# Optimization experiments

Hardware: AMD Instinct MI355X
Metric: run time of the kernel (lower is better)

## Reference

```python
import jax, jax.numpy as jnp
import numpy as np

W_BIT = 4
OUT_F = 11008
IN_F = 4096
K = 16


def unpack_sign(q_bytes):
    """q_bytes: [n_bytes] int32 holding uint8 values. Little-endian bit order.
    Returns float32 signs in {-1, +1} of shape [OUT_F, IN_F]."""
    bits = (q_bytes[:, None] >> jnp.arange(8, dtype=q_bytes.dtype)) & 1  # [n_bytes, 8]
    signs = (2 * bits - 1).astype(jnp.float32)
    return signs.reshape(OUT_F, IN_F)


def setup_inputs() -> dict:
    key = jax.random.key(0)
    k0, k1, k2, k3 = jax.random.split(key, 4)
    x = jax.random.normal(k0, (4, 2048, IN_F), dtype=jnp.float32)
    # packed sign bits: one byte stores 8 signs; OUT_F*IN_F//8 bytes per bit-plane
    qweight = jax.random.randint(k1, (W_BIT, OUT_F * IN_F // 8), 0, 256, dtype=jnp.int32)
    u = jax.random.normal(k2, (W_BIT, OUT_F, K), dtype=jnp.float32) * 0.05
    vt = jax.random.normal(k3, (W_BIT, K, IN_F), dtype=jnp.float32) * 0.05
    return {"x": x, "qweight": qweight, "u": u, "vt": vt}


def reference(x, qweight, u, vt):
    # Reconstruct full weight: w = sum_i sign_i * (u_i @ vt_i), then GEMM x @ w.T.
    # Loop over the small fixed w_bit count to avoid holding all [OUT,IN] bit-planes at once.
    w = jnp.zeros((OUT_F, IN_F), dtype=x.dtype)
    for i in range(W_BIT):
        signs = unpack_sign(qweight[i])            # [OUT_F, IN_F]
        w = w + signs * (u[i] @ vt[i])             # rank-K reconstruction masked by signs
    return x @ w.T                                  # [B, S, OUT_F]
```

## Files before the change

kernel.cpp:

```cpp
#include <hip/hip_runtime.h>
#include <hip/hip_bf16.h>

#define W_BIT 4
#define OUT_F 11008
#define IN_F 4096
#define KRANK 16
#define M_DIM 8192
#define QW_PLANE (OUT_F * IN_F / 8)

#define N_DIM OUT_F
#define K_DIM IN_F
#define NT 64
#define NBN 43

typedef __attribute__((ext_vector_type(8))) short short8;
typedef __attribute__((ext_vector_type(4))) float f32x4;

__device__ __forceinline__ short f2bf(float f) {
    union { float f; unsigned u; } v;
    v.f = f;
    unsigned r = v.u + 0x7fffu + ((v.u >> 16) & 1u);
    return (short)(r >> 16);
}

__device__ __forceinline__ void async16(void* lds, const void* g) {
    __builtin_amdgcn_global_load_lds(
        (const __attribute__((address_space(1))) unsigned int*)g,
        (__attribute__((address_space(3))) unsigned int*)lds,
        16, 0, 0);
}

#define BAR() __builtin_amdgcn_s_barrier()
#define LGKM0() do { asm volatile("s_waitcnt lgkmcnt(0)" ::: "memory"); \
                     __builtin_amdgcn_sched_barrier(0); } while (0)
#define VM8() asm volatile("s_waitcnt vmcnt(8)" ::: "memory")
#define VM0() asm volatile("s_waitcnt vmcnt(0)" ::: "memory")
#define PRIO1() __builtin_amdgcn_s_setprio(1)
#define PRIO0() __builtin_amdgcn_s_setprio(0)
#define SBAR0() __builtin_amdgcn_sched_barrier(0)

__global__ __launch_bounds__(256) void convert_x_kernel(
    const float* __restrict__ x, short* __restrict__ xb) {
    int tid = blockIdx.x * blockDim.x + threadIdx.x;
    int stride = gridDim.x * blockDim.x;
    const int n8 = (M_DIM * IN_F) / 8;
    for (int i = tid; i < n8; i += stride) {
        f32x4 a = ((const f32x4*)x)[2 * i];
        f32x4 b = ((const f32x4*)x)[2 * i + 1];
        short8 o;
        o[0] = f2bf(a[0]); o[1] = f2bf(a[1]); o[2] = f2bf(a[2]); o[3] = f2bf(a[3]);
        o[4] = f2bf(b[0]); o[5] = f2bf(b[1]); o[6] = f2bf(b[2]); o[7] = f2bf(b[3]);
        ((short8*)xb)[i] = o;
    }
}

__global__ __launch_bounds__(256) void reconstruct_w_kernel(
    const int* __restrict__ qw, const float* __restrict__ u,
    const float* __restrict__ vt, short* __restrict__ wb) {
    __shared__ float vts[W_BIT][KRANK][128];
    __shared__ float us[W_BIT][KRANK][64];

    const int t = threadIdx.x;
    const int o0 = blockIdx.y * 64;
    const int c0 = blockIdx.x * 128;

    for (int idx = t; idx < W_BIT * KRANK * 128; idx += 256) {
        int i = idx >> 11;
        int rem = idx & 2047;
        int k = rem >> 7;
        int c = rem & 127;
        vts[i][k][c] = vt[(i * KRANK + k) * IN_F + c0 + c];
    }
    for (int idx = t; idx < W_BIT * KRANK * 64; idx += 256) {
        int i = idx >> 10;
        int rem = idx & 1023;
        int o = rem >> 4;
        int k = rem & 15;
        us[i][k][o] = u[((size_t)i * OUT_F + o0 + o) * KRANK + k];
    }
    __syncthreads();

    const int to = (t >> 4) * 4;
    const int tc = (t & 15) * 8;

    float wacc[4][8];
#pragma unroll
    for (int r = 0; r < 4; ++r)
#pragma unroll
        for (int c = 0; c < 8; ++c) wacc[r][c] = 0.f;

#pragma unroll
    for (int i = 0; i < W_BIT; ++i) {
        float dot[4][8];
#pragma unroll
        for (int r = 0; r < 4; ++r)
#pragma unroll
            for (int c = 0; c < 8; ++c) dot[r][c] = 0.f;

#pragma unroll
        for (int k = 0; k < KRANK; ++k) {
            f32x4 uv = *(const f32x4*)&us[i][k][to];
            f32x4 v0 = *(const f32x4*)&vts[i][k][tc];
            f32x4 v1 = *(const f32x4*)&vts[i][k][tc + 4];
#pragma unroll
            for (int r = 0; r < 4; ++r) {
#pragma unroll
                for (int c = 0; c < 4; ++c) {
                    dot[r][c]     += uv[r] * v0[c];
                    dot[r][c + 4] += uv[r] * v1[c];
                }
            }
        }
#pragma unroll
        for (int r = 0; r < 4; ++r) {
            unsigned byte = (unsigned)qw[i * QW_PLANE + (((o0 + to + r) * IN_F + c0 + tc) >> 3)];
#pragma unroll
            for (int c = 0; c < 8; ++c) {
                wacc[r][c] += ((byte >> c) & 1u) ? dot[r][c] : -dot[r][c];
            }
        }
    }

#pragma unroll
    for (int r = 0; r < 4; ++r) {
        short8 o8;
#pragma unroll
        for (int c = 0; c < 8; ++c) o8[c] = f2bf(wacc[r][c]);
        *(short8*)&wb[(size_t)(o0 + to + r) * IN_F + c0 + tc] = o8;
    }
}

__global__ __launch_bounds__(512, 2) void gemm256_kernel(
    const short* __restrict__ A, const short* __restrict__ B, float* __restrict__ C) {
    extern __shared__ short lds[];

    const int t = threadIdx.x;
    const int lane = t & 63, wid = t >> 6;
    const int wr = wid >> 2, wc = wid & 3;
    const int fr = lane & 15, fq = lane >> 4;

    const int bid = blockIdx.x;
    const int cpx = gridDim.x >> 3;
    const int swz = (bid & 7) * cpx + (bid >> 3);
    const int bm = swz / NBN, bn = swz % NBN;
    const long row0 = (long)bm * 256, col0 = (long)bn * 256;

    const int srow_b = t >> 3;
    const int scol = (((t & 7) ^ ((t >> 3) & 7)) << 3);
    const short* gA = A + (row0 + srow_b) * K_DIM + scol;
    const short* gB = B + (col0 + srow_b) * K_DIM + scol;
    const int ldst = t * 8;

    const int arow = (wr * 128 + fr) * 64;
    const int brow = (wc * 64 + fr) * 64;
    const int cswz = (fr & 7) << 3;
    const int colk0  = (fq << 3) ^ cswz;
    const int colk32 = (32 | (fq << 3)) ^ cswz;

    f32x4 acc[8][4];
#pragma unroll
    for (int m = 0; m < 8; ++m)
#pragma unroll
        for (int n = 0; n < 4; ++n) acc[m][n] = (f32x4)0.f;

    short8 af0[8], af1[8], bf0[4], bf1[4];

#define STAGE4(gp, base, ktcol)                                        \
    _Pragma("unroll") for (int l = 0; l < 4; ++l)                      \
        async16(&lds[(base) + ldst + l * 4096],                        \
                (gp) + (size_t)l * 64 * K_DIM + (ktcol))

#define LDA8(dst, base, colk)                                          \
    _Pragma("unroll") for (int m = 0; m < 8; ++m)                      \
        dst[m] = *(const short8*)&lds[(base) + arow + m * 1024 + (colk)]

#define LDB1(dst, n, base, colk)                                       \
    dst[n] = *(const short8*)&lds[(base) + 16384 + brow + (n) * 1024 + (colk)]

#define MF2(A8, B4, nlo)                                               \
    _Pragma("unroll") for (int m = 0; m < 8; ++m) {                    \
        acc[m][nlo] = __builtin_amdgcn_mfma_f32_16x16x32_bf16(         \
            A8[m], B4[nlo], acc[m][nlo], 0, 0, 0);                     \
        acc[m][(nlo) + 1] = __builtin_amdgcn_mfma_f32_16x16x32_bf16(   \
            A8[m], B4[(nlo) + 1], acc[m][(nlo) + 1], 0, 0, 0);         \
    }

    STAGE4(gA, 0, 0);
    STAGE4(gB, 16384, 0);
    STAGE4(gA, 32768, 64);
    STAGE4(gB, 32768 + 16384, 64);
    VM8();
    BAR();
    LDA8(af0, 0, colk0);
    LDB1(bf0, 0, 0, colk0); LDB1(bf0, 1, 0, colk0);
    LDB1(bf0, 2, 0, colk0); LDB1(bf0, 3, 0, colk0);

    for (int g = 0; g < NT; ++g) {
        const int ab  = (g & 1) * 32768;
        const int ab2 = ((g & 1) ^ 1) * 32768;
        const bool st2 = (g + 2 < NT);
        const bool rd1 = (g + 1 < NT);
        const size_t kt2 = (size_t)(g + 2) * 64;

        LDA8(af1, ab, colk32);
        LDB1(bf1, 0, ab, colk32);
        LDB1(bf1, 1, ab, colk32);
        BAR();
        LGKM0();
        PRIO1(); MF2(af0, bf0, 0); PRIO0();
        SBAR0();
        BAR();

        if (st2) STAGE4(gA, ab, kt2);
        LDB1(bf1, 2, ab, colk32);
        LDB1(bf1, 3, ab, colk32);
        BAR();
        LGKM0();
        PRIO1(); MF2(af0, bf0, 2); PRIO0();
        SBAR0();
        BAR();

        if (st2) STAGE4(gB, ab + 16384, kt2);
        BAR();
        PRIO1(); MF2(af1, bf1, 0); PRIO0();
        if (st2) { VM8(); } else { VM0(); }
        SBAR0();
        BAR();

        if (rd1) {
            LDA8(af0, ab2, colk0);
            LDB1(bf0, 0, ab2, colk0); LDB1(bf0, 1, ab2, colk0);
            LDB1(bf0, 2, ab2, colk0); LDB1(bf0, 3, ab2, colk0);
        }
        BAR();
        LGKM0();
        PRIO1(); MF2(af1, bf1, 2); PRIO0();
        SBAR0();
        BAR();
    }

#pragma unroll
    for (int m = 0; m < 8; ++m) {
#pragma unroll
        for (int n = 0; n < 4; ++n) {
            f32x4 v = acc[m][n];
            long r0 = row0 + wr * 128 + m * 16 + fq * 4;
            long cc = col0 + wc * 64 + n * 16 + fr;
#pragma unroll
            for (int jj = 0; jj < 4; ++jj)
                C[(size_t)(r0 + jj) * N_DIM + cc] = v[jj];
        }
    }
#undef STAGE4
#undef LDA8
#undef LDB1
#undef MF2
}

extern "C" void kernel_launch(void* const* d_in, const int* in_sizes, int n_in,
                              void* d_out, int out_size, void* d_ws, size_t ws_size,
                              hipStream_t stream) {
    const float* x  = (const float*)d_in[0];
    const int*   qw = (const int*)d_in[1];
    const float* u  = (const float*)d_in[2];
    const float* vt = (const float*)d_in[3];
    float* out = (float*)d_out;

    const size_t wb_bytes = (size_t)OUT_F * IN_F * 2;
    short* wb = (short*)d_ws;
    short* xb = (short*)((char*)d_ws + wb_bytes);

    (void)hipFuncSetAttribute((const void*)gemm256_kernel,
                              hipFuncAttributeMaxDynamicSharedMemorySize, 131072);

    hipLaunchKernelGGL(convert_x_kernel, dim3(2048), dim3(256), 0, stream, x, xb);
    hipLaunchKernelGGL(reconstruct_w_kernel, dim3(IN_F / 128, OUT_F / 64), dim3(256), 0, stream,
                       qw, u, vt, wb);
    hipLaunchKernelGGL(gemm256_kernel, dim3((M_DIM / 256) * (N_DIM / 256)), dim3(512), 131072,
                       stream, xb, wb, out);
}
```

Before: 915.9 us.

## Restructure GEMM main loop into quadrant MFMA phases with staggered A/B prefetch

Reorganizes the bf16 GEMM inner loop into four phases, each issuing a 4x4 MFMA quadrant from smaller A and B register fragments. A is now prefetched one tile ahead into the other LDS buffer and B two tiles ahead. LDS waits use partial lgkmcnt counts instead of full drains, so fragment loads for the next phase overlap the current MFMAs. The goal is better overlap of LDS reads and global-to-LDS copies with the matrix units. In exchange, the asymmetric buffer timing adds hazard risk if the vmcnt and lgkmcnt counts are wrong.

```diff
diff --git a/kernel.cpp b/kernel.cpp
--- a/kernel.cpp
+++ b/kernel.cpp
@@ -31,13 +31,13 @@
 }
 
 #define BAR() __builtin_amdgcn_s_barrier()
-#define LGKM0() do { asm volatile("s_waitcnt lgkmcnt(0)" ::: "memory"); \
+#define SBAR0() __builtin_amdgcn_sched_barrier(0)
+#define LGKM(n) do { asm volatile("s_waitcnt lgkmcnt(" #n ")" ::: "memory"); \
                      __builtin_amdgcn_sched_barrier(0); } while (0)
-#define VM8() asm volatile("s_waitcnt vmcnt(8)" ::: "memory")
-#define VM0() asm volatile("s_waitcnt vmcnt(0)" ::: "memory")
+#define VMC(n) do { asm volatile("s_waitcnt vmcnt(" #n ")" ::: "memory"); \
+                    __builtin_amdgcn_sched_barrier(0); } while (0)
 #define PRIO1() __builtin_amdgcn_s_setprio(1)
 #define PRIO0() __builtin_amdgcn_s_setprio(0)
-#define SBAR0() __builtin_amdgcn_sched_barrier(0)
 
 __global__ __launch_bounds__(256) void convert_x_kernel(
     const float* __restrict__ x, short* __restrict__ xb) {
@@ -163,78 +163,75 @@
 #pragma unroll
         for (int n = 0; n < 4; ++n) acc[m][n] = (f32x4)0.f;
 
-    short8 af0[8], af1[8], bf0[4], bf1[4];
+    short8 af[4][4], bf[2][4];
 
 #define STAGE4(gp, base, ktcol)                                        \
     _Pragma("unroll") for (int l = 0; l < 4; ++l)                      \
         async16(&lds[(base) + ldst + l * 4096],                        \
                 (gp) + (size_t)l * 64 * K_DIM + (ktcol))
 
-#define LDA8(dst, base, colk)                                          \
-    _Pragma("unroll") for (int m = 0; m < 8; ++m)                      \
-        dst[m] = *(const short8*)&lds[(base) + arow + m * 1024 + (colk)]
-
-#define LDB1(dst, n, base, colk)                                       \
-    dst[n] = *(const short8*)&lds[(base) + 16384 + brow + (n) * 1024 + (colk)]
-
-#define MF2(A8, B4, nlo)                                               \
-    _Pragma("unroll") for (int m = 0; m < 8; ++m) {                    \
-        acc[m][nlo] = __builtin_amdgcn_mfma_f32_16x16x32_bf16(         \
-            A8[m], B4[nlo], acc[m][nlo], 0, 0, 0);                     \
-        acc[m][(nlo) + 1] = __builtin_amdgcn_mfma_f32_16x16x32_bf16(   \
-            A8[m], B4[(nlo) + 1], acc[m][(nlo) + 1], 0, 0, 0);         \
-    }
+#define LDA4(j, base, mh, colk)                                        \
+    _Pragma("unroll") for (int m = 0; m < 4; ++m)                      \
+        af[j][m] = *(const short8*)&lds[(base) + arow + (mh) * 4096 + m * 1024 + (colk)]
+
+#define LDB4(j, base, colk)                                            \
+    _Pragma("unroll") for (int n = 0; n < 4; ++n)                      \
+        bf[j][n] = *(const short8*)&lds[(base) + 16384 + brow + n * 1024 + (colk)]
+
+#define MFQ(j, jb, mbase)                                              \
+    _Pragma("unroll") for (int m = 0; m < 4; ++m)                      \
+        _Pragma("unroll") for (int n = 0; n < 4; ++n)                  \
+            acc[(mbase) + m][n] = __builtin_amdgcn_mfma_f32_16x16x32_bf16( \
+                af[j][m], bf[jb][n], acc[(mbase) + m][n], 0, 0, 0)
 
     STAGE4(gA, 0, 0);
     STAGE4(gB, 16384, 0);
-    STAGE4(gA, 32768, 64);
     STAGE4(gB, 32768 + 16384, 64);
-    VM8();
+    VMC(4);
     BAR();
-    LDA8(af0, 0, colk0);
-    LDB1(bf0, 0, 0, colk0); LDB1(bf0, 1, 0, colk0);
-    LDB1(bf0, 2, 0, colk0); LDB1(bf0, 3, 0, colk0);
+    LDA4(0, 0, 0, colk0);
+    LDB4(0, 0, colk0);
 
     for (int g = 0; g < NT; ++g) {
-        const int ab  = (g & 1) * 32768;
-        const int ab2 = ((g & 1) ^ 1) * 32768;
-        const bool st2 = (g + 2 < NT);
-        const bool rd1 = (g + 1 < NT);
-        const size_t kt2 = (size_t)(g + 2) * 64;
-
-        LDA8(af1, ab, colk32);
-        LDB1(bf1, 0, ab, colk32);
-        LDB1(bf1, 1, ab, colk32);
-        BAR();
-        LGKM0();
-        PRIO1(); MF2(af0, bf0, 0); PRIO0();
-        SBAR0();
-        BAR();
-
-        if (st2) STAGE4(gA, ab, kt2);
-        LDB1(bf1, 2, ab, colk32);
-        LDB1(bf1, 3, ab, colk32);
-        BAR();
-        LGKM0();
-        PRIO1(); MF2(af0, bf0, 2); PRIO0();
-        SBAR0();
-        BAR();
-
-        if (st2) STAGE4(gB, ab + 16384, kt2);
-        BAR();
-        PRIO1(); MF2(af1, bf1, 0); PRIO0();
-        if (st2) { VM8(); } else { VM0(); }
-        SBAR0();
-        BAR();
-
-        if (rd1) {
-            LDA8(af0, ab2, colk0);
-            LDB1(bf0, 0, ab2, colk0); LDB1(bf0, 1, ab2, colk0);
-            LDB1(bf0, 2, ab2, colk0); LDB1(bf0, 3, ab2, colk0);
-        }
-        BAR();
-        LGKM0();
-        PRIO1(); MF2(af1, bf1, 2); PRIO0();
+        const int cur = (g & 1) * 32768;
+        const int oth = 32768 - cur;
+        const bool h1 = (g + 1 < NT);
+        const bool h2 = (g + 2 < NT);
+
+        if (h1) STAGE4(gA, oth, (size_t)(g + 1) * 64);
+        LDA4(1, cur, 1, colk0);
+        BAR();
+        LGKM(4);
+        PRIO1(); MFQ(0, 0, 0); PRIO0();
+        SBAR0();
+        BAR();
+
+        LDA4(2, cur, 0, colk32);
+        LDB4(1, cur, colk32);
+        BAR();
+        LGKM(8);
+        PRIO1(); MFQ(1, 0, 4); PRIO0();
+        SBAR0();
+        BAR();
+
+        LDA4(3, cur, 1, colk32);
+        BAR();
+        LGKM(4);
+        PRIO1(); MFQ(2, 1, 0); PRIO0();
+        SBAR0();
+        BAR();
+
+        if (h2) STAGE4(gB, cur + 16384, (size_t)(g + 2) * 64);
+        if (h2) { VMC(4); } else { VMC(0); }
+        BAR();
+        if (h1) {
+            LDA4(0, oth, 0, colk0);
+            LDB4(0, oth, colk0);
+            LGKM(8);
+        } else {
+            LGKM(0);
+        }
+        PRIO1(); MFQ(3, 1, 4); PRIO0();
         SBAR0();
         BAR();
     }
@@ -252,9 +249,9 @@
         }
     }
 #undef STAGE4
-#undef LDA8
-#undef LDB1
-#undef MF2
+#undef LDA4
+#undef LDB4
+#undef MFQ
 }
 
 extern "C" void kernel_launch(void* const* d_in, const int* in_sizes, int n_in,
```

After: 901.0 us. No clear change (-1.6%).
